# Kernel tuning notes

Measured on AMD Instinct MI355X. Metric: run time of the kernel, lower is better.

## Reference

```python
import jax, jax.numpy as jnp
import numpy as np

DILATIONS = (1, 2, 4, 8, 16, 32, 64, 128, 256)
R = 128          # residual/skip channels
K = 3            # kernel size
B, CIN, T = 8, 1, 16384
COUT = 1
L = len(DILATIONS)


def causal_conv(x, w, b, dilation):
    # x: [B, Cin, T], w: [Cout, Cin, K] -> [B, Cout, T], left-padded (causal)
    k = w.shape[-1]
    pad = dilation * (k - 1)
    y = jax.lax.conv_general_dilated(
        x, w, window_strides=(1,), padding=[(pad, 0)],
        rhs_dilation=(dilation,), dimension_numbers=("NCH", "OIH", "NCH"))
    return y + b[None, :, None]


def setup_inputs() -> dict:
    key = jax.random.key(0)
    ks = jax.random.split(key, 11)
    s = 0.1  # weight scale to keep gated activations in a healthy range
    return {
        "x": jax.random.normal(ks[0], (B, CIN, T), jnp.float32),
        "input_w": s * jax.random.normal(ks[1], (R, CIN, 1), jnp.float32),
        "input_b": s * jax.random.normal(ks[2], (R,), jnp.float32),
        "conv_w": s * jax.random.normal(ks[3], (L, 2 * R, R, K), jnp.float32),
        "conv_b": s * jax.random.normal(ks[4], (L, 2 * R), jnp.float32),
        "out_w": s * jax.random.normal(ks[5], (L, R, R, 1), jnp.float32),
        "out_b": s * jax.random.normal(ks[6], (L, R), jnp.float32),
        "output1_w": s * jax.random.normal(ks[7], (R, R * L, 1), jnp.float32),
        "output1_b": s * jax.random.normal(ks[8], (R,), jnp.float32),
        "output2_w": s * jax.random.normal(ks[9], (COUT, R, 1), jnp.float32),
        "output2_b": s * jax.random.normal(ks[10], (COUT,), jnp.float32),
    }


def reference(x, input_w, input_b, conv_w, conv_b, out_w, out_b,
              output1_w, output1_b, output2_w, output2_b):
    # input layer: 1x1 conv + tanh (use_output_transform=False)
    h = jnp.tanh(causal_conv(x, input_w, input_b, 1))

    skips = []
    for i, d in enumerate(DILATIONS):
        pre = causal_conv(h, conv_w[i], conv_b[i], d)      # [B, 2R, T]
        t, g = jnp.split(pre, 2, axis=1)
        z = jnp.tanh(t) * jax.nn.sigmoid(g)                # gated activation
        skips.append(z)                                     # skip = activation out
        res = causal_conv(z, out_w[i], out_b[i], 1)         # 1x1 output transform
        h = h + res                                         # residual connection

    sk = jnp.concatenate(skips, axis=1)                     # [B, R*L, T]
    y = jnp.tanh(causal_conv(sk, output1_w, output1_b, 1))
    out = causal_conv(y, output2_w, output2_b, 1)           # linear
    return out
```

## Files before the change

kernel.cpp:

```cpp
#include <hip/hip_runtime.h>
#include <cstdint>
#include <cstddef>

#define T_LEN 16384
#define BATCH 8
#define NLAYER 9

typedef _Float16 f16;
typedef __attribute__((ext_vector_type(8))) _Float16 f16x8;
typedef __attribute__((ext_vector_type(4))) float f32x4;
#define MFMA_F16 __builtin_amdgcn_mfma_f32_16x16x32_f16

__device__ __forceinline__ void stage16(const f16* g, f16* l) {
    __builtin_amdgcn_global_load_lds(
        (const __attribute__((address_space(1))) unsigned int*)g,
        (__attribute__((address_space(3))) unsigned int*)l, 16, 0, 0);
}

__device__ __forceinline__ float fast_tanh(float x) {
    return 1.0f - 2.0f / (__expf(2.0f * x) + 1.0f);
}

__global__ __launch_bounds__(256) void prep_weights(
    const float* __restrict__ cw, const float* __restrict__ ow,
    const float* __restrict__ o1w, f16* __restrict__ wA, f16* __restrict__ wB)
{
    int n = blockIdx.x * 256 + threadIdx.x;
    const int NA = NLAYER * 12 * 256 * 32;
    const int NB = NLAYER * 4 * 256 * 32;
    if (n < NA) {
        int kp = n & 31; int q = n >> 5;
        int c = q & 255; q >>= 8;
        int ch = q % 12; int l = q / 12;
        int i = kp >> 3, j = kp & 7;
        int il = i ^ ((c >> 1) & 3);
        int kpl = il * 8 + j;
        int tap = ch >> 2;
        int r = (ch & 3) * 32 + kpl;
        wA[n] = (f16)cw[((size_t)(l * 256 + c) * 128 + r) * 3 + tap];
    } else if (n < NA + NB) {
        int m = n - NA;
        int kp = m & 31; int q = m >> 5;
        int c = q & 255; q >>= 8;
        int ch = q & 3; int l = q >> 2;
        int k = ch * 32 + kp;
        float v = (c < 128) ? ow[(size_t)(l * 128 + c) * 128 + k]
                            : o1w[(size_t)(c - 128) * 1152 + l * 128 + k];
        wB[m] = (f16)v;
    }
}

__global__ __launch_bounds__(256) void input_init(
    const float* __restrict__ x, const float* __restrict__ iw,
    const float* __restrict__ ib,
    f16* __restrict__ h, f16* __restrict__ acc1)
{
    int n = blockIdx.x * 256 + threadIdx.x;
    int r = n & 127; int bt = n >> 7;
    h[n] = (f16)fast_tanh(iw[r] * x[bt] + ib[r]);
    acc1[n] = (f16)0.0f;
}

__global__ __launch_bounds__(256, 4) void layer_kernel(
    const f16* __restrict__ h_in, f16* __restrict__ h_out,
    f16* __restrict__ acc1,
    const f16* __restrict__ wA,
    const f16* __restrict__ wB,
    const float* __restrict__ cb,
    const float* __restrict__ ob,
    int d)
{
    __shared__ __align__(16) char smem_raw[34816];
    f16* const Bsm = (f16*)smem_raw;
    f16* const zsR = (f16*)smem_raw;
    f16* const zsS = (f16*)smem_raw + 8704;

    const int tid  = threadIdx.x;
    const int lane = tid & 63;
    const int w4   = tid >> 6;
    const int mg   = w4 & 1;
    const int ng   = w4 >> 1;
    const int col  = lane & 15;
    const int quad = lane >> 4;
    const int b    = blockIdx.y;
    const int bx   = blockIdx.x;
    const int xt   = ((bx & 7) << 5) | (bx >> 3);
    const int t0   = xt * 64;

    const f16* hb = h_in + (size_t)b * T_LEN * 128;
    const int bswz = (quad ^ ((col >> 1) & 3)) * 8;

    f32x4 acc[2][8];
#pragma unroll
    for (int mt = 0; mt < 2; ++mt)
#pragma unroll
        for (int nt = 0; nt < 8; ++nt) acc[mt][nt] = (f32x4)0.0f;

    f16x8 a[2][4];
    auto loadA = [&](int tap) {
        const int off = (2 - tap) * d;
#pragma unroll
        for (int mt = 0; mt < 2; ++mt) {
            int t = t0 + mg * 32 + mt * 16 + col - off;
            int tc = t < 0 ? 0 : t;
            const f16* hp = &hb[(size_t)tc * 128 + quad * 8];
#pragma unroll
            for (int cc = 0; cc < 4; ++cc) {
                f16x8 v = *(const f16x8*)&hp[cc * 32];
                a[mt][cc] = (t >= 0) ? v : (f16x8)(f16)0.0f;
            }
        }
    };

    {
        const f16* s0 = wA + w4 * 1024 + lane * 8;
        f16* d0 = Bsm + w4 * 1024;
        stage16(s0, d0); stage16(s0 + 512, d0 + 512);
        const f16* s1 = wA + 4096 + w4 * 1024 + lane * 8;
        f16* d1 = Bsm + 4096 + w4 * 1024;
        stage16(s1, d1); stage16(s1 + 512, d1 + 512);
        __builtin_amdgcn_sched_barrier(0);
        loadA(0);
        __builtin_amdgcn_sched_barrier(0);
        asm volatile("s_waitcnt vmcnt(10)" ::: "memory");
        __builtin_amdgcn_s_barrier();
        __builtin_amdgcn_sched_barrier(0);
    }

#pragma unroll
    for (int hc = 0; hc < 24; ++hc) {
        if (hc == 8) loadA(1);
        if (hc == 16) loadA(2);
        if (hc + 2 < 24) {
            const f16* s = wA + (hc + 2) * 4096 + w4 * 1024 + lane * 8;
            f16* dd = Bsm + ((hc + 2) & 3) * 4096 + w4 * 1024;
            stage16(s, dd); stage16(s + 512, dd + 512);
        }
        const f16* bsc = Bsm + (hc & 3) * 4096;
        const int c = (hc >> 1) & 3;
        const int nbase = (hc & 1) * 4;
#pragma unroll
        for (int ntl = 0; ntl < 4; ++ntl) {
            int row = ng * 64 + ntl * 16 + col;
            f16x8 bf = *(const f16x8*)&bsc[row * 32 + bswz];
            acc[0][nbase + ntl] = MFMA_F16(a[0][c], bf, acc[0][nbase + ntl], 0, 0, 0);
            acc[1][nbase + ntl] = MFMA_F16(a[1][c], bf, acc[1][nbase + ntl], 0, 0, 0);
        }
        __builtin_amdgcn_sched_barrier(0);
        if (hc == 22) {
            asm volatile("s_waitcnt vmcnt(0)" ::: "memory");
        } else if (hc < 22) {
            asm volatile("s_waitcnt vmcnt(2)" ::: "memory");
        }
        if (hc < 23) __builtin_amdgcn_s_barrier();
        __builtin_amdgcn_sched_barrier(0);
    }
    __syncthreads();

#pragma unroll
    for (int nt = 0; nt < 4; ++nt) {
        int j = ng * 64 + nt * 16 + col;
        float cf = cb[j];
        float cg = cb[j + 128];
#pragma unroll
        for (int mt = 0; mt < 2; ++mt)
#pragma unroll
            for (int reg = 0; reg < 4; ++reg) {
                float f = acc[mt][nt][reg]     + cf;
                float g = acc[mt][nt + 4][reg] + cg;
                float E = __builtin_amdgcn_exp2f(2.885390082f * f);
                float S = __builtin_amdgcn_exp2f(1.442695041f * g);
                float z = (E - 1.0f) * S *
                          __builtin_amdgcn_rcpf((E + 1.0f) * (S + 1.0f));
                zsR[(mg * 32 + mt * 16 + quad * 4 + reg) * 136 + j] = (f16)z;
            }
    }
    __syncthreads();

#pragma unroll
    for (int mt = 0; mt < 2; ++mt)
#pragma unroll
        for (int nt = 0; nt < 8; ++nt) acc[mt][nt] = (f32x4)0.0f;

#pragma unroll
    for (int ch = 0; ch < 4; ++ch) {
        f16x8 a2[2];
#pragma unroll
        for (int mt = 0; mt < 2; ++mt)
            a2[mt] = *(const f16x8*)&zsR[(mg * 32 + mt * 16 + col) * 136 + ch * 32 + quad * 8];
        const f16* wc = wB + ch * 8192;
#pragma unroll
        for (int nt = 0; nt < 8; ++nt) {
            int nb = (nt < 4) ? (ng * 64 + nt * 16)
                              : (128 + ng * 64 + (nt - 4) * 16);
            f16x8 bf = *(const f16x8*)&wc[(nb + col) * 32 + quad * 8];
            acc[0][nt] = MFMA_F16(a2[0], bf, acc[0][nt], 0, 0, 0);
            acc[1][nt] = MFMA_F16(a2[1], bf, acc[1][nt], 0, 0, 0);
        }
    }
    __syncthreads();

#pragma unroll
    for (int nt = 0; nt < 4; ++nt) {
        int n = ng * 64 + nt * 16 + col;
        float o = ob[n];
#pragma unroll
        for (int mt = 0; mt < 2; ++mt)
#pragma unroll
            for (int reg = 0; reg < 4; ++reg) {
                int r = (mg * 32 + mt * 16 + quad * 4 + reg) * 136 + n;
                zsR[r] = (f16)(acc[mt][nt][reg] + o);
                zsS[r] = (f16)acc[mt][nt + 4][reg];
            }
    }
    __syncthreads();
    const int orow = tid >> 2, oseg = tid & 3;
    const size_t gb = (size_t)b * T_LEN * 128 + (size_t)(t0 + orow) * 128 + oseg * 32;
    f16x8 hv[4], av[4];
#pragma unroll
    for (int i = 0; i < 4; ++i) hv[i] = *(const f16x8*)&h_in[gb + i * 8];
#pragma unroll
    for (int i = 0; i < 4; ++i) av[i] = *(const f16x8*)&acc1[gb + i * 8];
#pragma unroll
    for (int i = 0; i < 4; ++i) {
        f16x8 rv = *(const f16x8*)&zsR[orow * 136 + oseg * 32 + i * 8];
        *(f16x8*)&h_out[gb + i * 8] = hv[i] + rv;
    }
#pragma unroll
    for (int i = 0; i < 4; ++i) {
        f16x8 sv = *(const f16x8*)&zsS[orow * 136 + oseg * 32 + i * 8];
        *(f16x8*)&acc1[gb + i * 8] = av[i] + sv;
    }
}

__global__ __launch_bounds__(256) void final_kernel(
    const f16* __restrict__ acc1, const float* __restrict__ b1,
    const float* __restrict__ w2, const float* __restrict__ b2,
    float* __restrict__ out)
{
    int lane = threadIdx.x & 63;
    int w = threadIdx.x >> 6;
    int bt = blockIdx.x * 4 + w;
    float v0 = (float)acc1[(size_t)bt * 128 + lane];
    float v1 = (float)acc1[(size_t)bt * 128 + lane + 64];
    float s = w2[lane] * fast_tanh(v0 + b1[lane]) +
              w2[lane + 64] * fast_tanh(v1 + b1[lane + 64]);
#pragma unroll
    for (int k = 1; k < 64; k <<= 1) s += __shfl_xor(s, k, 64);
    if (lane == 0) out[bt] = s + b2[0];
}

extern "C" void kernel_launch(void* const* d_in, const int* in_sizes, int n_in,
                              void* d_out, int out_size, void* d_ws, size_t ws_size,
                              hipStream_t stream)
{
    const float* x   = (const float*)d_in[0];
    const float* iw  = (const float*)d_in[1];
    const float* ib  = (const float*)d_in[2];
    const float* cw  = (const float*)d_in[3];
    const float* cb  = (const float*)d_in[4];
    const float* ow  = (const float*)d_in[5];
    const float* ob  = (const float*)d_in[6];
    const float* o1w = (const float*)d_in[7];
    const float* o1b = (const float*)d_in[8];
    const float* o2w = (const float*)d_in[9];
    const float* o2b = (const float*)d_in[10];
    float* out = (float*)d_out;

    const size_t HTR = (size_t)BATCH * T_LEN * 128;
    f16* hA   = (f16*)d_ws;
    f16* hB   = hA + HTR;
    f16* acc1 = hB + HTR;
    f16* wAp  = acc1 + HTR;
    f16* wBp  = wAp + (size_t)NLAYER * 12 * 256 * 32;

    prep_weights<<<4608, 256, 0, stream>>>(cw, ow, o1w, wAp, wBp);
    input_init<<<65536, 256, 0, stream>>>(x, iw, ib, hA, acc1);

    const int DIL[NLAYER] = {1, 2, 4, 8, 16, 32, 64, 128, 256};
    f16* hin = hA; f16* hout = hB;
    for (int l = 0; l < NLAYER; ++l) {
        layer_kernel<<<dim3(T_LEN / 64, BATCH), 256, 0, stream>>>(
            hin, hout, acc1,
            wAp + (size_t)l * 12 * 256 * 32, wBp + (size_t)l * 4 * 256 * 32,
            cb + l * 256, ob + l * 128, DIL[l]);
        f16* tmp = hin; hin = hout; hout = tmp;
    }
    final_kernel<<<BATCH * T_LEN / 4, 256, 0, stream>>>(acc1, o1b, o2w, o2b, out);
}
```

Baseline: 754.8 us.

## Split layer kernel across 8 waves with smaller per-wave N tiles

New measurement: 936.7 us. 1.24x slower.

```diff
diff --git a/kernel.cpp b/kernel.cpp
--- a/kernel.cpp
+++ b/kernel.cpp
@@ -61,7 +61,7 @@
     acc1[n] = (f16)0.0f;
 }
 
-__global__ __launch_bounds__(256, 4) void layer_kernel(
+__global__ __launch_bounds__(512, 6) void layer_kernel(
     const f16* __restrict__ h_in, f16* __restrict__ h_out,
     f16* __restrict__ acc1,
     const f16* __restrict__ wA,
@@ -77,9 +77,9 @@
 
     const int tid  = threadIdx.x;
     const int lane = tid & 63;
-    const int w4   = tid >> 6;
-    const int mg   = w4 & 1;
-    const int ng   = w4 >> 1;
+    const int w    = tid >> 6;
+    const int mg   = w >> 2;
+    const int nq   = w & 3;
     const int col  = lane & 15;
     const int quad = lane >> 4;
     const int b    = blockIdx.y;
@@ -89,12 +89,13 @@
 
     const f16* hb = h_in + (size_t)b * T_LEN * 128;
     const int bswz = (quad ^ ((col >> 1) & 3)) * 8;
-
-    f32x4 acc[2][8];
+    const int lrow = nq * 32 + col;
+
+    f32x4 acc[2][4];
 #pragma unroll
     for (int mt = 0; mt < 2; ++mt)
 #pragma unroll
-        for (int nt = 0; nt < 8; ++nt) acc[mt][nt] = (f32x4)0.0f;
+        for (int nt = 0; nt < 4; ++nt) acc[mt][nt] = (f32x4)0.0f;
 
     f16x8 a[2][4];
     auto loadA = [&](int tap) {
@@ -113,44 +114,43 @@
     };
 
     {
-        const f16* s0 = wA + w4 * 1024 + lane * 8;
-        f16* d0 = Bsm + w4 * 1024;
-        stage16(s0, d0); stage16(s0 + 512, d0 + 512);
-        const f16* s1 = wA + 4096 + w4 * 1024 + lane * 8;
-        f16* d1 = Bsm + 4096 + w4 * 1024;
-        stage16(s1, d1); stage16(s1 + 512, d1 + 512);
-        __builtin_amdgcn_sched_barrier(0);
         loadA(0);
         __builtin_amdgcn_sched_barrier(0);
-        asm volatile("s_waitcnt vmcnt(10)" ::: "memory");
+        stage16(wA + tid * 8,        Bsm + tid * 8);
+        stage16(wA + 4096 + tid * 8, Bsm + 4096 + tid * 8);
+        stage16(wA + 8192 + tid * 8, Bsm + 8192 + tid * 8);
+        __builtin_amdgcn_sched_barrier(0);
+        asm volatile("s_waitcnt vmcnt(2)" ::: "memory");
         __builtin_amdgcn_s_barrier();
         __builtin_amdgcn_sched_barrier(0);
     }
 
 #pragma unroll
     for (int hc = 0; hc < 24; ++hc) {
-        if (hc == 8) loadA(1);
+        if (hc == 8)  loadA(1);
         if (hc == 16) loadA(2);
-        if (hc + 2 < 24) {
-            const f16* s = wA + (hc + 2) * 4096 + w4 * 1024 + lane * 8;
-            f16* dd = Bsm + ((hc + 2) & 3) * 4096 + w4 * 1024;
-            stage16(s, dd); stage16(s + 512, dd + 512);
-        }
+        __builtin_amdgcn_sched_barrier(0);
+        if (hc + 3 < 24) {
+            stage16(wA + (hc + 3) * 4096 + tid * 8,
+                    Bsm + ((hc + 3) & 3) * 4096 + tid * 8);
+        }
+        __builtin_amdgcn_sched_barrier(0);
         const f16* bsc = Bsm + (hc & 3) * 4096;
-        const int c = (hc >> 1) & 3;
-        const int nbase = (hc & 1) * 4;
-#pragma unroll
-        for (int ntl = 0; ntl < 4; ++ntl) {
-            int row = ng * 64 + ntl * 16 + col;
-            f16x8 bf = *(const f16x8*)&bsc[row * 32 + bswz];
-            acc[0][nbase + ntl] = MFMA_F16(a[0][c], bf, acc[0][nbase + ntl], 0, 0, 0);
-            acc[1][nbase + ntl] = MFMA_F16(a[1][c], bf, acc[1][nbase + ntl], 0, 0, 0);
-        }
-        __builtin_amdgcn_sched_barrier(0);
-        if (hc == 22) {
+        const int kc  = (hc >> 1) & 3;
+        const int ntb = (hc & 1) * 2;
+#pragma unroll
+        for (int ntl = 0; ntl < 2; ++ntl) {
+            f16x8 bf = *(const f16x8*)&bsc[(lrow + ntl * 16) * 32 + bswz];
+            acc[0][ntb + ntl] = MFMA_F16(a[0][kc], bf, acc[0][ntb + ntl], 0, 0, 0);
+            acc[1][ntb + ntl] = MFMA_F16(a[1][kc], bf, acc[1][ntb + ntl], 0, 0, 0);
+        }
+        __builtin_amdgcn_sched_barrier(0);
+        if (hc < 21) {
+            asm volatile("s_waitcnt vmcnt(2)" ::: "memory");
+        } else if (hc == 21) {
+            asm volatile("s_waitcnt vmcnt(1)" ::: "memory");
+        } else if (hc == 22) {
             asm volatile("s_waitcnt vmcnt(0)" ::: "memory");
-        } else if (hc < 22) {
-            asm volatile("s_waitcnt vmcnt(2)" ::: "memory");
         }
         if (hc < 23) __builtin_amdgcn_s_barrier();
         __builtin_amdgcn_sched_barrier(0);
@@ -158,8 +158,8 @@
     __syncthreads();
 
 #pragma unroll
-    for (int nt = 0; nt < 4; ++nt) {
-        int j = ng * 64 + nt * 16 + col;
+    for (int nt = 0; nt < 2; ++nt) {
+        int j = nq * 32 + nt * 16 + col;
         float cf = cb[j];
         float cg = cb[j + 128];
 #pragma unroll
@@ -167,7 +167,7 @@
 #pragma unroll
             for (int reg = 0; reg < 4; ++reg) {
                 float f = acc[mt][nt][reg]     + cf;
-                float g = acc[mt][nt + 4][reg] + cg;
+                float g = acc[mt][nt + 2][reg] + cg;
                 float E = __builtin_amdgcn_exp2f(2.885390082f * f);
                 float S = __builtin_amdgcn_exp2f(1.442695041f * g);
                 float z = (E - 1.0f) * S *
@@ -180,20 +180,19 @@
 #pragma unroll
     for (int mt = 0; mt < 2; ++mt)
 #pragma unroll
-        for (int nt = 0; nt < 8; ++nt) acc[mt][nt] = (f32x4)0.0f;
-
+        for (int nt = 0; nt < 4; ++nt) acc[mt][nt] = (f32x4)0.0f;
+
+    const f16* wBb = wB + (size_t)(nq * 32 + col) * 32 + quad * 8;
 #pragma unroll
     for (int ch = 0; ch < 4; ++ch) {
         f16x8 a2[2];
 #pragma unroll
         for (int mt = 0; mt < 2; ++mt)
             a2[mt] = *(const f16x8*)&zsR[(mg * 32 + mt * 16 + col) * 136 + ch * 32 + quad * 8];
-        const f16* wc = wB + ch * 8192;
-#pragma unroll
-        for (int nt = 0; nt < 8; ++nt) {
-            int nb = (nt < 4) ? (ng * 64 + nt * 16)
-                              : (128 + ng * 64 + (nt - 4) * 16);
-            f16x8 bf = *(const f16x8*)&wc[(nb + col) * 32 + quad * 8];
+        const f16* bp = wBb + ch * 8192;
+#pragma unroll
+        for (int nt = 0; nt < 4; ++nt) {
+            f16x8 bf = *(const f16x8*)&bp[(nt & 1) * 512 + (nt >> 1) * 4096];
             acc[0][nt] = MFMA_F16(a2[0], bf, acc[0][nt], 0, 0, 0);
             acc[1][nt] = MFMA_F16(a2[1], bf, acc[1][nt], 0, 0, 0);
         }
@@ -201,8 +200,8 @@
     __syncthreads();
 
 #pragma unroll
-    for (int nt = 0; nt < 4; ++nt) {
-        int n = ng * 64 + nt * 16 + col;
+    for (int nt = 0; nt < 2; ++nt) {
+        int n = nq * 32 + nt * 16 + col;
         float o = ob[n];
 #pragma unroll
         for (int mt = 0; mt < 2; ++mt)
@@ -210,25 +209,25 @@
             for (int reg = 0; reg < 4; ++reg) {
                 int r = (mg * 32 + mt * 16 + quad * 4 + reg) * 136 + n;
                 zsR[r] = (f16)(acc[mt][nt][reg] + o);
-                zsS[r] = (f16)acc[mt][nt + 4][reg];
+                zsS[r] = (f16)acc[mt][nt + 2][reg];
             }
     }
     __syncthreads();
-    const int orow = tid >> 2, oseg = tid & 3;
-    const size_t gb = (size_t)b * T_LEN * 128 + (size_t)(t0 + orow) * 128 + oseg * 32;
-    f16x8 hv[4], av[4];
-#pragma unroll
-    for (int i = 0; i < 4; ++i) hv[i] = *(const f16x8*)&h_in[gb + i * 8];
-#pragma unroll
-    for (int i = 0; i < 4; ++i) av[i] = *(const f16x8*)&acc1[gb + i * 8];
-#pragma unroll
-    for (int i = 0; i < 4; ++i) {
-        f16x8 rv = *(const f16x8*)&zsR[orow * 136 + oseg * 32 + i * 8];
+    const int orow = tid >> 3, oseg = tid & 7;
+    const size_t gb = (size_t)b * T_LEN * 128 + (size_t)(t0 + orow) * 128 + oseg * 16;
+    f16x8 hv[2], av[2];
+#pragma unroll
+    for (int i = 0; i < 2; ++i) hv[i] = *(const f16x8*)&h_in[gb + i * 8];
+#pragma unroll
+    for (int i = 0; i < 2; ++i) av[i] = *(const f16x8*)&acc1[gb + i * 8];
+#pragma unroll
+    for (int i = 0; i < 2; ++i) {
+        f16x8 rv = *(const f16x8*)&zsR[orow * 136 + oseg * 16 + i * 8];
         *(f16x8*)&h_out[gb + i * 8] = hv[i] + rv;
     }
 #pragma unroll
-    for (int i = 0; i < 4; ++i) {
-        f16x8 sv = *(const f16x8*)&zsS[orow * 136 + oseg * 32 + i * 8];
+    for (int i = 0; i < 2; ++i) {
+        f16x8 sv = *(const f16x8*)&zsS[orow * 136 + oseg * 16 + i * 8];
         *(f16x8*)&acc1[gb + i * 8] = av[i] + sv;
     }
 }
@@ -280,7 +279,7 @@
     const int DIL[NLAYER] = {1, 2, 4, 8, 16, 32, 64, 128, 256};
     f16* hin = hA; f16* hout = hB;
     for (int l = 0; l < NLAYER; ++l) {
-        layer_kernel<<<dim3(T_LEN / 64, BATCH), 256, 0, stream>>>(
+        layer_kernel<<<dim3(T_LEN / 64, BATCH), 512, 0, stream>>>(
             hin, hout, acc1,
             wAp + (size_t)l * 12 * 256 * 32, wBp + (size_t)l * 4 * 256 * 32,
             cb + l * 256, ob + l * 128, DIL[l]);
```

## Deepen weight prefetch, spread activation loads, and hoist epilogue global reads

Applied to the files above, without the earlier changes.

New measurement: 749.3 us. About the same (-0.7%).

```diff
diff --git a/kernel.cpp b/kernel.cpp
--- a/kernel.cpp
+++ b/kernel.cpp
@@ -97,65 +97,81 @@
         for (int nt = 0; nt < 8; ++nt) acc[mt][nt] = (f32x4)0.0f;
 
     f16x8 a[2][4];
-    auto loadA = [&](int tap) {
+    auto loadA_cc = [&](int tap, int cc) {
         const int off = (2 - tap) * d;
 #pragma unroll
         for (int mt = 0; mt < 2; ++mt) {
             int t = t0 + mg * 32 + mt * 16 + col - off;
             int tc = t < 0 ? 0 : t;
-            const f16* hp = &hb[(size_t)tc * 128 + quad * 8];
-#pragma unroll
-            for (int cc = 0; cc < 4; ++cc) {
-                f16x8 v = *(const f16x8*)&hp[cc * 32];
-                a[mt][cc] = (t >= 0) ? v : (f16x8)(f16)0.0f;
-            }
+            f16x8 v = *(const f16x8*)&hb[(size_t)tc * 128 + quad * 8 + cc * 32];
+            a[mt][cc] = (t >= 0) ? v : (f16x8)(f16)0.0f;
         }
     };
 
     {
-        const f16* s0 = wA + w4 * 1024 + lane * 8;
-        f16* d0 = Bsm + w4 * 1024;
-        stage16(s0, d0); stage16(s0 + 512, d0 + 512);
-        const f16* s1 = wA + 4096 + w4 * 1024 + lane * 8;
-        f16* d1 = Bsm + 4096 + w4 * 1024;
-        stage16(s1, d1); stage16(s1 + 512, d1 + 512);
-        __builtin_amdgcn_sched_barrier(0);
-        loadA(0);
-        __builtin_amdgcn_sched_barrier(0);
-        asm volatile("s_waitcnt vmcnt(10)" ::: "memory");
+#pragma unroll
+        for (int cc = 0; cc < 4; ++cc) loadA_cc(0, cc);
+        __builtin_amdgcn_sched_barrier(0);
+#pragma unroll
+        for (int hh = 0; hh < 3; ++hh) {
+            const f16* s = wA + hh * 4096 + w4 * 1024 + lane * 8;
+            f16* dd = Bsm + hh * 4096 + w4 * 1024;
+            stage16(s, dd); stage16(s + 512, dd + 512);
+        }
+        __builtin_amdgcn_sched_barrier(0);
+        asm volatile("s_waitcnt vmcnt(4)" ::: "memory");
         __builtin_amdgcn_s_barrier();
         __builtin_amdgcn_sched_barrier(0);
     }
 
 #pragma unroll
     for (int hc = 0; hc < 24; ++hc) {
-        if (hc == 8) loadA(1);
-        if (hc == 16) loadA(2);
-        if (hc + 2 < 24) {
-            const f16* s = wA + (hc + 2) * 4096 + w4 * 1024 + lane * 8;
-            f16* dd = Bsm + ((hc + 2) & 3) * 4096 + w4 * 1024;
+        if (hc >= 2 && hc <= 16 && (hc & 1) == 0) {
+            const int tap = (hc <= 8) ? 1 : 2;
+            const int cc  = (hc <= 8) ? ((hc - 2) >> 1) : ((hc - 10) >> 1);
+            loadA_cc(tap, cc);
+        }
+        __builtin_amdgcn_sched_barrier(0);
+        if (hc + 3 < 24) {
+            const f16* s = wA + (hc + 3) * 4096 + w4 * 1024 + lane * 8;
+            f16* dd = Bsm + ((hc + 3) & 3) * 4096 + w4 * 1024;
             stage16(s, dd); stage16(s + 512, dd + 512);
         }
+        __builtin_amdgcn_sched_barrier(0);
         const f16* bsc = Bsm + (hc & 3) * 4096;
-        const int c = (hc >> 1) & 3;
+        const int kc    = (hc >> 1) & 3;
         const int nbase = (hc & 1) * 4;
 #pragma unroll
         for (int ntl = 0; ntl < 4; ++ntl) {
             int row = ng * 64 + ntl * 16 + col;
             f16x8 bf = *(const f16x8*)&bsc[row * 32 + bswz];
-            acc[0][nbase + ntl] = MFMA_F16(a[0][c], bf, acc[0][nbase + ntl], 0, 0, 0);
-            acc[1][nbase + ntl] = MFMA_F16(a[1][c], bf, acc[1][nbase + ntl], 0, 0, 0);
-        }
-        __builtin_amdgcn_sched_barrier(0);
-        if (hc == 22) {
+            acc[0][nbase + ntl] = MFMA_F16(a[0][kc], bf, acc[0][nbase + ntl], 0, 0, 0);
+            acc[1][nbase + ntl] = MFMA_F16(a[1][kc], bf, acc[1][nbase + ntl], 0, 0, 0);
+        }
+        __builtin_amdgcn_sched_barrier(0);
+        if (hc <= 1) {
+            asm volatile("s_waitcnt vmcnt(4)" ::: "memory");
+        } else if (hc <= 17) {
+            asm volatile("s_waitcnt vmcnt(6)" ::: "memory");
+        } else if (hc <= 20) {
+            asm volatile("s_waitcnt vmcnt(4)" ::: "memory");
+        } else if (hc == 21) {
+            asm volatile("s_waitcnt vmcnt(2)" ::: "memory");
+        } else if (hc == 22) {
             asm volatile("s_waitcnt vmcnt(0)" ::: "memory");
-        } else if (hc < 22) {
-            asm volatile("s_waitcnt vmcnt(2)" ::: "memory");
         }
         if (hc < 23) __builtin_amdgcn_s_barrier();
         __builtin_amdgcn_sched_barrier(0);
     }
     __syncthreads();
+
+    f16x8 b0[8];
+#pragma unroll
+    for (int nt = 0; nt < 8; ++nt) {
+        int nb = (nt < 4) ? (ng * 64 + nt * 16)
+                          : (128 + ng * 64 + (nt - 4) * 16);
+        b0[nt] = *(const f16x8*)&wB[(size_t)(nb + col) * 32 + quad * 8];
+    }
 
 #pragma unroll
     for (int nt = 0; nt < 4; ++nt) {
@@ -193,11 +209,21 @@
         for (int nt = 0; nt < 8; ++nt) {
             int nb = (nt < 4) ? (ng * 64 + nt * 16)
                               : (128 + ng * 64 + (nt - 4) * 16);
-            f16x8 bf = *(const f16x8*)&wc[(nb + col) * 32 + quad * 8];
+            f16x8 bf = (ch == 0) ? b0[nt]
+                                 : *(const f16x8*)&wc[(nb + col) * 32 + quad * 8];
             acc[0][nt] = MFMA_F16(a2[0], bf, acc[0][nt], 0, 0, 0);
             acc[1][nt] = MFMA_F16(a2[1], bf, acc[1][nt], 0, 0, 0);
         }
     }
+
+    const int orow = tid >> 2, oseg = tid & 3;
+    const size_t gb = (size_t)b * T_LEN * 128 + (size_t)(t0 + orow) * 128 + oseg * 32;
+    f16x8 hv[4], av[4];
+#pragma unroll
+    for (int i = 0; i < 4; ++i) hv[i] = *(const f16x8*)&h_in[gb + i * 8];
+#pragma unroll
+    for (int i = 0; i < 4; ++i) av[i] = *(const f16x8*)&acc1[gb + i * 8];
+
     __syncthreads();
 
 #pragma unroll
@@ -214,13 +240,6 @@
             }
     }
     __syncthreads();
-    const int orow = tid >> 2, oseg = tid & 3;
-    const size_t gb = (size_t)b * T_LEN * 128 + (size_t)(t0 + orow) * 128 + oseg * 32;
-    f16x8 hv[4], av[4];
-#pragma unroll
-    for (int i = 0; i < 4; ++i) hv[i] = *(const f16x8*)&h_in[gb + i * 8];
-#pragma unroll
-    for (int i = 0; i < 4; ++i) av[i] = *(const f16x8*)&acc1[gb + i * 8];
 #pragma unroll
     for (int i = 0; i < 4; ++i) {
         f16x8 rv = *(const f16x8*)&zsR[orow * 136 + oseg * 32 + i * 8];
```

## Software-pipeline LDS fragment reads ahead of MFMAs and hoist epilogue global loads

Applied to the files above, without the earlier changes.

Result: no change. 765.5 us (+1.4%).

```diff
diff --git a/kernel.cpp b/kernel.cpp
--- a/kernel.cpp
+++ b/kernel.cpp
@@ -10,6 +10,7 @@
 typedef __attribute__((ext_vector_type(8))) _Float16 f16x8;
 typedef __attribute__((ext_vector_type(4))) float f32x4;
 #define MFMA_F16 __builtin_amdgcn_mfma_f32_16x16x32_f16
+#define PIN() __builtin_amdgcn_sched_barrier(0)
 
 __device__ __forceinline__ void stage16(const f16* g, f16* l) {
     __builtin_amdgcn_global_load_lds(
@@ -47,6 +48,8 @@
         float v = (c < 128) ? ow[(size_t)(l * 128 + c) * 128 + k]
                             : o1w[(size_t)(c - 128) * 1152 + l * 128 + k];
         wB[m] = (f16)v;
+    } else if (n < NA + NB + 128) {
+        wB[n - NA] = (f16)0.0f;
     }
 }
 
@@ -61,11 +64,12 @@
     acc1[n] = (f16)0.0f;
 }
 
-__global__ __launch_bounds__(256, 4) void layer_kernel(
+__global__ __launch_bounds__(256, 3) void layer_kernel(
     const f16* __restrict__ h_in, f16* __restrict__ h_out,
     f16* __restrict__ acc1,
     const f16* __restrict__ wA,
     const f16* __restrict__ wB,
+    const f16* __restrict__ zpad,
     const float* __restrict__ cb,
     const float* __restrict__ ob,
     int d)
@@ -102,60 +106,91 @@
 #pragma unroll
         for (int mt = 0; mt < 2; ++mt) {
             int t = t0 + mg * 32 + mt * 16 + col - off;
-            int tc = t < 0 ? 0 : t;
-            const f16* hp = &hb[(size_t)tc * 128 + quad * 8];
-#pragma unroll
-            for (int cc = 0; cc < 4; ++cc) {
-                f16x8 v = *(const f16x8*)&hp[cc * 32];
-                a[mt][cc] = (t >= 0) ? v : (f16x8)(f16)0.0f;
-            }
+            const f16* base = (t >= 0) ? &hb[(size_t)t * 128] : zpad;
+#pragma unroll
+            for (int cc = 0; cc < 4; ++cc)
+                a[mt][cc] = *(const f16x8*)&base[quad * 8 + cc * 32];
         }
     };
 
+    f16x8 fr[2][4];
+
     {
-        const f16* s0 = wA + w4 * 1024 + lane * 8;
-        f16* d0 = Bsm + w4 * 1024;
-        stage16(s0, d0); stage16(s0 + 512, d0 + 512);
-        const f16* s1 = wA + 4096 + w4 * 1024 + lane * 8;
-        f16* d1 = Bsm + 4096 + w4 * 1024;
-        stage16(s1, d1); stage16(s1 + 512, d1 + 512);
-        __builtin_amdgcn_sched_barrier(0);
+#pragma unroll
+        for (int hh = 0; hh < 2; ++hh) {
+            const f16* s = wA + hh * 4096 + w4 * 1024 + lane * 8;
+            f16* dd = Bsm + hh * 4096 + w4 * 1024;
+            stage16(s, dd); stage16(s + 512, dd + 512);
+        }
+        PIN();
         loadA(0);
-        __builtin_amdgcn_sched_barrier(0);
+        PIN();
         asm volatile("s_waitcnt vmcnt(10)" ::: "memory");
         __builtin_amdgcn_s_barrier();
-        __builtin_amdgcn_sched_barrier(0);
+        PIN();
     }
 
 #pragma unroll
     for (int hc = 0; hc < 24; ++hc) {
-        if (hc == 8) loadA(1);
-        if (hc == 16) loadA(2);
         if (hc + 2 < 24) {
             const f16* s = wA + (hc + 2) * 4096 + w4 * 1024 + lane * 8;
             f16* dd = Bsm + ((hc + 2) & 3) * 4096 + w4 * 1024;
             stage16(s, dd); stage16(s + 512, dd + 512);
         }
-        const f16* bsc = Bsm + (hc & 3) * 4096;
-        const int c = (hc >> 1) & 3;
-        const int nbase = (hc & 1) * 4;
-#pragma unroll
-        for (int ntl = 0; ntl < 4; ++ntl) {
-            int row = ng * 64 + ntl * 16 + col;
-            f16x8 bf = *(const f16x8*)&bsc[row * 32 + bswz];
-            acc[0][nbase + ntl] = MFMA_F16(a[0][c], bf, acc[0][nbase + ntl], 0, 0, 0);
-            acc[1][nbase + ntl] = MFMA_F16(a[1][c], bf, acc[1][nbase + ntl], 0, 0, 0);
-        }
-        __builtin_amdgcn_sched_barrier(0);
-        if (hc == 22) {
+        PIN();
+        {
+            const f16* bsc = Bsm + (hc & 3) * 4096;
+#pragma unroll
+            for (int ntl = 0; ntl < 4; ++ntl) {
+                int row = ng * 64 + ntl * 16 + col;
+                fr[hc & 1][ntl] = *(const f16x8*)&bsc[row * 32 + bswz];
+            }
+        }
+        PIN();
+        if (hc > 0) {
+            const int c     = hc - 1;
+            const int kc    = (c >> 1) & 3;
+            const int nbase = (c & 1) * 4;
+            __builtin_amdgcn_s_setprio(1);
+#pragma unroll
+            for (int ntl = 0; ntl < 4; ++ntl) {
+                acc[0][nbase + ntl] = MFMA_F16(a[0][kc], fr[c & 1][ntl], acc[0][nbase + ntl], 0, 0, 0);
+                acc[1][nbase + ntl] = MFMA_F16(a[1][kc], fr[c & 1][ntl], acc[1][nbase + ntl], 0, 0, 0);
+            }
+            __builtin_amdgcn_s_setprio(0);
+        }
+        PIN();
+        if (hc == 8)  loadA(1);
+        if (hc == 16) loadA(2);
+        PIN();
+        if (hc == 0 || hc == 8 || hc == 16) {
+            asm volatile("s_waitcnt vmcnt(10)" ::: "memory");
+        } else if (hc == 22) {
             asm volatile("s_waitcnt vmcnt(0)" ::: "memory");
         } else if (hc < 22) {
             asm volatile("s_waitcnt vmcnt(2)" ::: "memory");
         }
         if (hc < 23) __builtin_amdgcn_s_barrier();
-        __builtin_amdgcn_sched_barrier(0);
+        PIN();
+    }
+    {
+        __builtin_amdgcn_s_setprio(1);
+#pragma unroll
+        for (int ntl = 0; ntl < 4; ++ntl) {
+            acc[0][4 + ntl] = MFMA_F16(a[0][3], fr[1][ntl], acc[0][4 + ntl], 0, 0, 0);
+            acc[1][4 + ntl] = MFMA_F16(a[1][3], fr[1][ntl], acc[1][4 + ntl], 0, 0, 0);
+        }
+        __builtin_amdgcn_s_setprio(0);
     }
     __syncthreads();
+
+    f16x8 b0[8];
+#pragma unroll
+    for (int nt = 0; nt < 8; ++nt) {
+        int nb = (nt < 4) ? (ng * 64 + nt * 16)
+                          : (128 + ng * 64 + (nt - 4) * 16);
+        b0[nt] = *(const f16x8*)&wB[(size_t)(nb + col) * 32 + quad * 8];
+    }
 
 #pragma unroll
     for (int nt = 0; nt < 4; ++nt) {
@@ -193,11 +228,21 @@
         for (int nt = 0; nt < 8; ++nt) {
             int nb = (nt < 4) ? (ng * 64 + nt * 16)
                               : (128 + ng * 64 + (nt - 4) * 16);
-            f16x8 bf = *(const f16x8*)&wc[(nb + col) * 32 + quad * 8];
+            f16x8 bf = (ch == 0) ? b0[nt]
+                                 : *(const f16x8*)&wc[(nb + col) * 32 + quad * 8];
             acc[0][nt] = MFMA_F16(a2[0], bf, acc[0][nt], 0, 0, 0);
             acc[1][nt] = MFMA_F16(a2[1], bf, acc[1][nt], 0, 0, 0);
         }
     }
+
+    const int orow = tid >> 2, oseg = tid & 3;
+    const size_t gb = (size_t)b * T_LEN * 128 + (size_t)(t0 + orow) * 128 + oseg * 32;
+    f16x8 hv[4], av[4];
+#pragma unroll
+    for (int i = 0; i < 4; ++i) hv[i] = *(const f16x8*)&h_in[gb + i * 8];
+#pragma unroll
+    for (int i = 0; i < 4; ++i) av[i] = *(const f16x8*)&acc1[gb + i * 8];
+
     __syncthreads();
 
 #pragma unroll
@@ -214,13 +259,6 @@
             }
     }
     __syncthreads();
-    const int orow = tid >> 2, oseg = tid & 3;
-    const size_t gb = (size_t)b * T_LEN * 128 + (size_t)(t0 + orow) * 128 + oseg * 32;
-    f16x8 hv[4], av[4];
-#pragma unroll
-    for (int i = 0; i < 4; ++i) hv[i] = *(const f16x8*)&h_in[gb + i * 8];
-#pragma unroll
-    for (int i = 0; i < 4; ++i) av[i] = *(const f16x8*)&acc1[gb + i * 8];
 #pragma unroll
     for (int i = 0; i < 4; ++i) {
         f16x8 rv = *(const f16x8*)&zsR[orow * 136 + oseg * 32 + i * 8];
@@ -273,8 +311,9 @@
     f16* acc1 = hB + HTR;
     f16* wAp  = acc1 + HTR;
     f16* wBp  = wAp + (size_t)NLAYER * 12 * 256 * 32;
-
-    prep_weights<<<4608, 256, 0, stream>>>(cw, ow, o1w, wAp, wBp);
+    f16* zpad = wBp + (size_t)NLAYER * 4 * 256 * 32;
+
+    prep_weights<<<4610, 256, 0, stream>>>(cw, ow, o1w, wAp, wBp);
     input_init<<<65536, 256, 0, stream>>>(x, iw, ib, hA, acc1);
 
     const int DIL[NLAYER] = {1, 2, 4, 8, 16, 32, 64, 128, 256};
@@ -283,7 +322,7 @@
         layer_kernel<<<dim3(T_LEN / 64, BATCH), 256, 0, stream>>>(
             hin, hout, acc1,
             wAp + (size_t)l * 12 * 256 * 32, wBp + (size_t)l * 4 * 256 * 32,
-            cb + l * 256, ob + l * 128, DIL[l]);
+            zpad, cb + l * 256, ob + l * 128, DIL[l]);
         f16* tmp = hin; hin = hout; hout = tmp;
     }
     final_kernel<<<BATCH * T_LEN / 4, 256, 0, stream>>>(acc1, o1b, o2w, o2b, out);
```
